# Kernel optimization log

Measured on AMD Instinct MI355X. Metric: run time of the kernel, lower is better.

The kernel has to match this reference:

```python
import jax, jax.numpy as jnp
import numpy as np

B, L, D, H = 2, 4096, 768, 12
HS = D // H  # head_size = 64
SCALE = HS ** -0.5


def setup_inputs() -> dict:
    key = jax.random.key(0)
    k1, k2, k3 = jax.random.split(key, 3)
    x = jax.random.normal(k1, (B, L, D), dtype=jnp.float32)
    # torch nn.Linear weights are [out_features, in_features]; y = x @ W.T
    Wq = jax.random.normal(k2, (D, D), dtype=jnp.float32) * (D ** -0.5)
    Wo = jax.random.normal(k3, (D, D), dtype=jnp.float32) * (D ** -0.5)
    return {"x": x, "Wq": Wq, "Wo": Wo}


def reference(x, Wq, Wo):
    b, l, d = x.shape
    # NOTE: source module uses self.query for Q, K, AND V (bug preserved).
    q = jnp.einsum('bld,ed->ble', x, Wq)              # [B,L,D]
    q = q.reshape(b, l, H, HS).transpose(0, 2, 1, 3)   # [B,H,L,HS]
    k = v = q                                          # K = V = Q (faithful)
    scores = jnp.einsum('bhqd,bhkd->bhqk', q, k) * SCALE  # [B,H,L,L]
    attn = jax.nn.softmax(scores, axis=-1)
    out = jnp.einsum('bhqk,bhkd->bhqd', attn, v)       # [B,H,L,HS]
    out = out.transpose(0, 2, 1, 3).reshape(b, l, d)   # [B,L,D]
    out = jnp.einsum('bld,ed->ble', out, Wo)           # output projection
    return out
```

## Files before the change

kernel.cpp:

```cpp
#include <hip/hip_runtime.h>
#include <hip/hip_bf16.h>

#define LQ 4096
#define DQ 768
#define NH 12
#define NB 2

typedef __attribute__((ext_vector_type(8))) short short8;
typedef __attribute__((ext_vector_type(4))) short short4v;
typedef __attribute__((ext_vector_type(2))) unsigned uint2v;
typedef __attribute__((ext_vector_type(4))) float f32x4;

__device__ __forceinline__ short f2bf(float f) {
    union { float f; unsigned u; } v; v.f = f;
    unsigned r = v.u + 0x7FFFu + ((v.u >> 16) & 1u);
    return (short)(r >> 16);
}

__device__ __forceinline__ unsigned pk2(float a, float b) {
    float2 t; t.x = a; t.y = b;
    __hip_bfloat162 h = __float22bfloat162_rn(t);
    unsigned u; __builtin_memcpy(&u, &h, 4);
    return u;
}

__device__ __forceinline__ f32x4 mfma16(short8 a, short8 b, f32x4 c) {
    return __builtin_amdgcn_mfma_f32_16x16x32_bf16(a, b, c, 0, 0, 0);
}

#define SQRT_C 0.424660f

__global__ __launch_bounds__(256) void cvtw(const float* __restrict__ a,
                                            short* __restrict__ o) {
    int i = blockIdx.x * 256 + threadIdx.x;
    float4 v = ((const float4*)a)[i];
    *(uint2v*)&o[i * 4] = (uint2v){pk2(v.x, v.y), pk2(v.z, v.w)};
}

template <int MODE>
__global__ __launch_bounds__(256, 3) void gemm_nt(const short* __restrict__ A,
                                                  const float* __restrict__ W,
                                                  void* __restrict__ Cp,
                                                  short* __restrict__ Qt) {
    __shared__ short As[128 * 72];
    __shared__ short Bs[64 * 72];
    const int t = threadIdx.x;
    const int lane = t & 63, w = t >> 6;
    const int lr = lane & 15, qd = lane >> 4;
    const int wm = (w & 1) * 64, wn = (w >> 1) * 32;
    const int lin = blockIdx.x;
    const int xcd = lin & 7, jj = lin >> 3;
    const int nt = jj % 12, mt = (jj / 12) * 8 + xcd;
    const int m0 = mt * 128, n0 = nt * 64;

    f32x4 acc[4][2];
#pragma unroll
    for (int i = 0; i < 4; ++i)
#pragma unroll
        for (int j = 0; j < 2; ++j) acc[i][j] = (f32x4){0.f, 0.f, 0.f, 0.f};

#pragma unroll
    for (int u = 0; u < 4; ++u) {
        int c = t + 256 * u, row = c >> 3, col = (c & 7) << 3;
        *(short8*)&As[row * 72 + col] = *(const short8*)&A[(size_t)(m0 + row) * DQ + col];
    }
#pragma unroll
    for (int u = 0; u < 4; ++u) {
        int c = t + 256 * u, row = c >> 4, col = (c & 15) << 2;
        float4 v = *(const float4*)&W[(size_t)(n0 + row) * DQ + col];
        *(uint2v*)&Bs[row * 72 + col] = (uint2v){pk2(v.x, v.y), pk2(v.z, v.w)};
    }
    __syncthreads();

    for (int kt = 0; kt < 12; ++kt) {
        short8 ra[4]; float4 rb[4];
        if (kt < 11) {
            const int k0 = (kt + 1) * 64;
#pragma unroll
            for (int u = 0; u < 4; ++u) {
                int c = t + 256 * u, row = c >> 3, col = (c & 7) << 3;
                ra[u] = *(const short8*)&A[(size_t)(m0 + row) * DQ + k0 + col];
            }
#pragma unroll
            for (int u = 0; u < 4; ++u) {
                int c = t + 256 * u, row = c >> 4, col = (c & 15) << 2;
                rb[u] = *(const float4*)&W[(size_t)(n0 + row) * DQ + k0 + col];
            }
        }
#pragma unroll
        for (int s = 0; s < 2; ++s) {
            short8 af[4], bf[2];
#pragma unroll
            for (int i = 0; i < 4; ++i)
                af[i] = *(short8*)&As[(wm + 16 * i + lr) * 72 + 32 * s + qd * 8];
#pragma unroll
            for (int j = 0; j < 2; ++j)
                bf[j] = *(short8*)&Bs[(wn + 16 * j + lr) * 72 + 32 * s + qd * 8];
#pragma unroll
            for (int i = 0; i < 4; ++i)
#pragma unroll
                for (int j = 0; j < 2; ++j)
                    acc[i][j] = mfma16(af[i], bf[j], acc[i][j]);
        }
        if (kt < 11) {
            __syncthreads();
#pragma unroll
            for (int u = 0; u < 4; ++u) {
                int c = t + 256 * u, row = c >> 3, col = (c & 7) << 3;
                *(short8*)&As[row * 72 + col] = ra[u];
            }
#pragma unroll
            for (int u = 0; u < 4; ++u) {
                int c = t + 256 * u, row = c >> 4, col = (c & 15) << 2;
                *(uint2v*)&Bs[row * 72 + col] = (uint2v){pk2(rb[u].x, rb[u].y), pk2(rb[u].z, rb[u].w)};
            }
            __syncthreads();
        }
    }

#pragma unroll
    for (int i = 0; i < 4; ++i)
#pragma unroll
        for (int j = 0; j < 2; ++j) {
            const int row0 = m0 + wm + 16 * i + qd * 4;
            const int col = n0 + wn + 16 * j + lr;
            if (MODE == 0) {
#pragma unroll
                for (int r = 0; r < 4; ++r)
                    ((float*)Cp)[(size_t)(row0 + r) * DQ + col] = acc[i][j][r];
            } else {
                const int b = row0 >> 12, l0 = row0 & 4095;
                const int h = col >> 6, hs = col & 63;
                const int bh = b * NH + h;
                short4v pk;
#pragma unroll
                for (int r = 0; r < 4; ++r) {
                    ((short*)Cp)[((size_t)bh * LQ + l0 + r) * 64 + hs] =
                        f2bf(acc[i][j][r] * SQRT_C);
                    pk[r] = f2bf(acc[i][j][r]);
                }
                *(short4v*)&Qt[((size_t)bh * 64 + hs) * LQ + l0] = pk;
            }
        }
}

__global__ __launch_bounds__(128, 2) void attn(const short* __restrict__ Q,
                                               const short* __restrict__ Qt,
                                               short* __restrict__ O) {
    const int linear = blockIdx.x;
    const int xcd = linear & 7, slot = linear >> 3;
    const int bh = 3 * xcd + (slot >> 5);
    const int qtile = slot & 31;
    const int t = threadIdx.x;
    const int lane = t & 63, w = t >> 6;
    const int lr = lane & 15, qd = lane >> 4;

    __shared__ short Ks[64 * 72];
    __shared__ short Vts[64 * 72];
    __shared__ short Ps[2][4][16 * 72];

    const short* Qbh = Q + (size_t)bh * LQ * 64;
    const short* Qtbh = Qt + (size_t)bh * 64 * LQ;
    const int q0 = qtile * 128 + w * 64;

    short8 aq[4][2];
#pragma unroll
    for (int i = 0; i < 4; ++i)
#pragma unroll
        for (int s = 0; s < 2; ++s)
            aq[i][s] = *(const short8*)&Qbh[(size_t)(q0 + 16 * i + lr) * 64 + 32 * s + qd * 8];

    f32x4 oacc[4][4];
#pragma unroll
    for (int i = 0; i < 4; ++i)
#pragma unroll
        for (int t2 = 0; t2 < 4; ++t2) oacc[i][t2] = (f32x4){0.f, 0.f, 0.f, 0.f};
    float l_st[4] = {0.f, 0.f, 0.f, 0.f};

#pragma unroll
    for (int u = 0; u < 4; ++u) {
        int cc = t + 128 * u;
        int row = cc >> 3, col = (cc & 7) << 3;
        *(short8*)&Ks[row * 72 + col] = *(const short8*)&Qbh[(size_t)row * 64 + col];
        *(short8*)&Vts[row * 72 + col] = *(const short8*)&Qtbh[(size_t)row * LQ + col];
    }
    __syncthreads();

    for (int kb = 0; kb < LQ / 64; ++kb) {
        short8 sk[4], sv[4];
        if (kb < LQ / 64 - 1) {
            const int k0 = (kb + 1) * 64;
#pragma unroll
            for (int u = 0; u < 4; ++u) {
                int cc = t + 128 * u;
                int row = cc >> 3, col = (cc & 7) << 3;
                sk[u] = *(const short8*)&Qbh[(size_t)(k0 + row) * 64 + col];
                sv[u] = *(const short8*)&Qtbh[(size_t)row * LQ + k0 + col];
            }
        }

        short8 kf[4][2];
#pragma unroll
        for (int t4 = 0; t4 < 4; ++t4)
#pragma unroll
            for (int s = 0; s < 2; ++s)
                kf[t4][s] = *(short8*)&Ks[(16 * t4 + lr) * 72 + 32 * s + qd * 8];

#pragma unroll
        for (int i = 0; i < 4; ++i) {
            f32x4 sacc[4];
#pragma unroll
            for (int t4 = 0; t4 < 4; ++t4) {
                sacc[t4] = (f32x4){0.f, 0.f, 0.f, 0.f};
#pragma unroll
                for (int s = 0; s < 2; ++s)
                    sacc[t4] = mfma16(kf[t4][s], aq[i][s], sacc[t4]);
            }
#pragma unroll
            for (int t4 = 0; t4 < 4; ++t4) {
                float p0 = __builtin_amdgcn_exp2f(sacc[t4][0]);
                float p1 = __builtin_amdgcn_exp2f(sacc[t4][1]);
                float p2 = __builtin_amdgcn_exp2f(sacc[t4][2]);
                float p3 = __builtin_amdgcn_exp2f(sacc[t4][3]);
                l_st[i] += (p0 + p1) + (p2 + p3);
                *(uint2v*)&Ps[w][i][lr * 72 + 16 * t4 + 4 * qd] =
                    (uint2v){pk2(p0, p1), pk2(p2, p3)};
            }
        }

#pragma unroll
        for (int ks = 0; ks < 2; ++ks) {
            short8 vb[4];
#pragma unroll
            for (int t2 = 0; t2 < 4; ++t2)
                vb[t2] = *(short8*)&Vts[(16 * t2 + lr) * 72 + 32 * ks + qd * 8];
#pragma unroll
            for (int i = 0; i < 4; ++i) {
                short8 pa = *(short8*)&Ps[w][i][lr * 72 + 32 * ks + qd * 8];
#pragma unroll
                for (int t2 = 0; t2 < 4; ++t2)
                    oacc[i][t2] = mfma16(pa, vb[t2], oacc[i][t2]);
            }
        }

        if (kb < LQ / 64 - 1) {
            __syncthreads();
#pragma unroll
            for (int u = 0; u < 4; ++u) {
                int cc = t + 128 * u;
                int row = cc >> 3, col = (cc & 7) << 3;
                *(short8*)&Ks[row * 72 + col] = sk[u];
                *(short8*)&Vts[row * 72 + col] = sv[u];
            }
            __syncthreads();
        }
    }

    const int b = bh / NH, h = bh % NH;
#pragma unroll
    for (int i = 0; i < 4; ++i) {
        float l = l_st[i];
        l += __shfl_xor(l, 16);
        l += __shfl_xor(l, 32);
        float inv[4];
#pragma unroll
        for (int r = 0; r < 4; ++r)
            inv[r] = 1.0f / __shfl(l, qd * 4 + r);
#pragma unroll
        for (int t2 = 0; t2 < 4; ++t2)
#pragma unroll
            for (int r = 0; r < 4; ++r) {
                int lq = q0 + 16 * i + qd * 4 + r;
                int e = h * 64 + 16 * t2 + lr;
                O[((size_t)(b * LQ + lq)) * DQ + e] = f2bf(oacc[i][t2][r] * inv[r]);
            }
    }
}

extern "C" void kernel_launch(void* const* d_in, const int* in_sizes, int n_in,
                              void* d_out, int out_size, void* d_ws, size_t ws_size,
                              hipStream_t stream) {
    (void)in_sizes; (void)n_in; (void)out_size; (void)ws_size;
    const float* x  = (const float*)d_in[0];
    const float* Wq = (const float*)d_in[1];
    const float* Wo = (const float*)d_in[2];
    float* out = (float*)d_out;

    const size_t NQ = (size_t)NB * NH * LQ * 64;
    short* Qws  = (short*)d_ws;
    short* Qtws = Qws  + NQ;
    short* Ows  = Qtws + NQ;

    cvtw<<<(NB * LQ * DQ) / 1024, 256, 0, stream>>>(x, Ows);
    gemm_nt<1><<<768, 256, 0, stream>>>(Ows, Wq, Qws, Qtws);
    attn<<<768, 128, 0, stream>>>(Qws, Qtws, Ows);
    gemm_nt<0><<<768, 256, 0, stream>>>(Ows, Wo, out, nullptr);
}
```

Before: 268.1 us.

## Pre-swizzle Q/V into MFMA fragment layout and drop LDS staging in attention

The Q-projection epilogue now stages its output through LDS and writes Q and V directly in MFMA-fragment-ordered blocks, replacing the row-major Q plus transposed Qt stores. The attention kernel loads K and V fragments straight from global memory into registers with a one-block prefetch of K, which removes the shared-memory K/V tiles and their two barriers per iteration. It also moves to 256 threads with 32 queries per wave, and the softmax scale is applied inside exp2 instead of being prescaled into Q. Every wave now fetches the full K/V blocks from global memory or L2 rather than sharing them through LDS, which raises cache traffic and register pressure.

```diff
diff --git a/kernel.cpp b/kernel.cpp
--- a/kernel.cpp
+++ b/kernel.cpp
@@ -7,7 +7,6 @@
 #define NB 2
 
 typedef __attribute__((ext_vector_type(8))) short short8;
-typedef __attribute__((ext_vector_type(4))) short short4v;
 typedef __attribute__((ext_vector_type(2))) unsigned uint2v;
 typedef __attribute__((ext_vector_type(4))) float f32x4;
 
@@ -28,8 +27,6 @@
     return __builtin_amdgcn_mfma_f32_16x16x32_bf16(a, b, c, 0, 0, 0);
 }
 
-#define SQRT_C 0.424660f
-
 __global__ __launch_bounds__(256) void cvtw(const float* __restrict__ a,
                                             short* __restrict__ o) {
     int i = blockIdx.x * 256 + threadIdx.x;
@@ -37,11 +34,12 @@
     *(uint2v*)&o[i * 4] = (uint2v){pk2(v.x, v.y), pk2(v.z, v.w)};
 }
 
+
 template <int MODE>
 __global__ __launch_bounds__(256, 3) void gemm_nt(const short* __restrict__ A,
                                                   const float* __restrict__ W,
                                                   void* __restrict__ Cp,
-                                                  short* __restrict__ Qt) {
+                                                  short* __restrict__ Vf) {
     __shared__ short As[128 * 72];
     __shared__ short Bs[64 * 72];
     const int t = threadIdx.x;
@@ -118,34 +116,65 @@
         }
     }
 
-#pragma unroll
-    for (int i = 0; i < 4; ++i)
-#pragma unroll
-        for (int j = 0; j < 2; ++j) {
-            const int row0 = m0 + wm + 16 * i + qd * 4;
-            const int col = n0 + wn + 16 * j + lr;
-            if (MODE == 0) {
+    if (MODE == 0) {
+#pragma unroll
+        for (int i = 0; i < 4; ++i)
+#pragma unroll
+            for (int j = 0; j < 2; ++j) {
+                const int row0 = m0 + wm + 16 * i + qd * 4;
+                const int col = n0 + wn + 16 * j + lr;
 #pragma unroll
                 for (int r = 0; r < 4; ++r)
                     ((float*)Cp)[(size_t)(row0 + r) * DQ + col] = acc[i][j][r];
-            } else {
-                const int b = row0 >> 12, l0 = row0 & 4095;
-                const int h = col >> 6, hs = col & 63;
-                const int bh = b * NH + h;
-                short4v pk;
+            }
+    } else {
+        short* Qf = (short*)Cp;
+        short* F = As;
+        const int bh = (m0 >> 12) * NH + nt;
+        const size_t gbase = (size_t)bh * (LQ * 64) + (size_t)(((m0 & 4095) >> 6) << 12);
+        __syncthreads();
+#pragma unroll
+        for (int i = 0; i < 4; ++i)
+#pragma unroll
+            for (int j = 0; j < 2; ++j) {
+                const int kl = wm + 16 * i + qd * 4;
+                const int hs = wn + 16 * j + lr;
+                const int fi = ((kl >> 6) << 12) + ((((hs >> 4) << 1) + ((kl >> 5) & 1)) << 9)
+                             + (((hs & 15) + (((kl >> 3) & 3) << 4)) << 3) + (kl & 7);
+                *(uint2v*)&F[fi] = (uint2v){pk2(acc[i][j][0], acc[i][j][1]),
+                                            pk2(acc[i][j][2], acc[i][j][3])};
+            }
+        __syncthreads();
+#pragma unroll
+        for (int p = 0; p < 4; ++p) {
+            int u = t + 256 * p;
+            *(short8*)&Vf[gbase + (size_t)u * 8] = *(short8*)&F[u * 8];
+        }
+        __syncthreads();
+#pragma unroll
+        for (int i = 0; i < 4; ++i)
+#pragma unroll
+            for (int j = 0; j < 2; ++j) {
+                const int hs = wn + 16 * j + lr;
 #pragma unroll
                 for (int r = 0; r < 4; ++r) {
-                    ((short*)Cp)[((size_t)bh * LQ + l0 + r) * 64 + hs] =
-                        f2bf(acc[i][j][r] * SQRT_C);
-                    pk[r] = f2bf(acc[i][j][r]);
+                    const int key = wm + 16 * i + qd * 4 + r;
+                    const int fi = ((key >> 6) << 12) + (((((key >> 4) & 3) << 1) + (hs >> 5)) << 9)
+                                 + (((qd * 4 + r) + (((hs >> 3) & 3) << 4)) << 3) + (hs & 7);
+                    F[fi] = f2bf(acc[i][j][r]);
                 }
-                *(short4v*)&Qt[((size_t)bh * 64 + hs) * LQ + l0] = pk;
-            }
-        }
-}
-
-__global__ __launch_bounds__(128, 2) void attn(const short* __restrict__ Q,
-                                               const short* __restrict__ Qt,
+            }
+        __syncthreads();
+#pragma unroll
+        for (int p = 0; p < 4; ++p) {
+            int u = t + 256 * p;
+            *(short8*)&Qf[gbase + (size_t)u * 8] = *(short8*)&F[u * 8];
+        }
+    }
+}
+
+__global__ __launch_bounds__(256, 3) void attn(const short* __restrict__ Qf,
+                                               const short* __restrict__ Vf,
                                                short* __restrict__ O) {
     const int linear = blockIdx.x;
     const int xcd = linear & 7, slot = linear >> 3;
@@ -155,59 +184,55 @@
     const int lane = t & 63, w = t >> 6;
     const int lr = lane & 15, qd = lane >> 4;
 
-    __shared__ short Ks[64 * 72];
-    __shared__ short Vts[64 * 72];
-    __shared__ short Ps[2][4][16 * 72];
-
-    const short* Qbh = Q + (size_t)bh * LQ * 64;
-    const short* Qtbh = Qt + (size_t)bh * 64 * LQ;
-    const int q0 = qtile * 128 + w * 64;
-
-    short8 aq[4][2];
-#pragma unroll
-    for (int i = 0; i < 4; ++i)
+    __shared__ short Ps[4][2][16 * 72];
+
+    const short* Qbh = Qf + (size_t)bh * (LQ * 64);
+    const short* Vbh = Vf + (size_t)bh * (LQ * 64);
+    const int q0 = qtile * 128 + w * 32;
+
+    short8 aq[2][2];
+#pragma unroll
+    for (int i = 0; i < 2; ++i) {
+        const int g = (q0 >> 4) + i;
 #pragma unroll
         for (int s = 0; s < 2; ++s)
-            aq[i][s] = *(const short8*)&Qbh[(size_t)(q0 + 16 * i + lr) * 64 + 32 * s + qd * 8];
-
-    f32x4 oacc[4][4];
-#pragma unroll
-    for (int i = 0; i < 4; ++i)
+            aq[i][s] = *(const short8*)&Qbh[g * 1024 + s * 512 + lane * 8];
+    }
+
+    f32x4 oacc[2][4];
+#pragma unroll
+    for (int i = 0; i < 2; ++i)
 #pragma unroll
         for (int t2 = 0; t2 < 4; ++t2) oacc[i][t2] = (f32x4){0.f, 0.f, 0.f, 0.f};
-    float l_st[4] = {0.f, 0.f, 0.f, 0.f};
-
-#pragma unroll
-    for (int u = 0; u < 4; ++u) {
-        int cc = t + 128 * u;
-        int row = cc >> 3, col = (cc & 7) << 3;
-        *(short8*)&Ks[row * 72 + col] = *(const short8*)&Qbh[(size_t)row * 64 + col];
-        *(short8*)&Vts[row * 72 + col] = *(const short8*)&Qtbh[(size_t)row * LQ + col];
-    }
-    __syncthreads();
+    float l_st[2] = {0.f, 0.f};
+
+    const float c = 0.125f * 1.44269504088896f;
+
+    short8 kf[4][2];
+#pragma unroll
+    for (int t4 = 0; t4 < 4; ++t4)
+#pragma unroll
+        for (int s = 0; s < 2; ++s)
+            kf[t4][s] = *(const short8*)&Qbh[(t4 * 2 + s) * 512 + lane * 8];
 
     for (int kb = 0; kb < LQ / 64; ++kb) {
-        short8 sk[4], sv[4];
+        short8 vb[4][2];
+#pragma unroll
+        for (int t2 = 0; t2 < 4; ++t2)
+#pragma unroll
+            for (int ks = 0; ks < 2; ++ks)
+                vb[t2][ks] = *(const short8*)&Vbh[kb * 4096 + (t2 * 2 + ks) * 512 + lane * 8];
+        short8 kfn[4][2];
         if (kb < LQ / 64 - 1) {
-            const int k0 = (kb + 1) * 64;
-#pragma unroll
-            for (int u = 0; u < 4; ++u) {
-                int cc = t + 128 * u;
-                int row = cc >> 3, col = (cc & 7) << 3;
-                sk[u] = *(const short8*)&Qbh[(size_t)(k0 + row) * 64 + col];
-                sv[u] = *(const short8*)&Qtbh[(size_t)row * LQ + k0 + col];
-            }
-        }
-
-        short8 kf[4][2];
-#pragma unroll
-        for (int t4 = 0; t4 < 4; ++t4)
-#pragma unroll
-            for (int s = 0; s < 2; ++s)
-                kf[t4][s] = *(short8*)&Ks[(16 * t4 + lr) * 72 + 32 * s + qd * 8];
-
-#pragma unroll
-        for (int i = 0; i < 4; ++i) {
+#pragma unroll
+            for (int t4 = 0; t4 < 4; ++t4)
+#pragma unroll
+                for (int s = 0; s < 2; ++s)
+                    kfn[t4][s] = *(const short8*)&Qbh[(kb + 1) * 4096 + (t4 * 2 + s) * 512 + lane * 8];
+        }
+
+#pragma unroll
+        for (int i = 0; i < 2; ++i) {
             f32x4 sacc[4];
 #pragma unroll
             for (int t4 = 0; t4 < 4; ++t4) {
@@ -218,47 +243,31 @@
             }
 #pragma unroll
             for (int t4 = 0; t4 < 4; ++t4) {
-                float p0 = __builtin_amdgcn_exp2f(sacc[t4][0]);
-                float p1 = __builtin_amdgcn_exp2f(sacc[t4][1]);
-                float p2 = __builtin_amdgcn_exp2f(sacc[t4][2]);
-                float p3 = __builtin_amdgcn_exp2f(sacc[t4][3]);
+                float p0 = __builtin_amdgcn_exp2f(sacc[t4][0] * c);
+                float p1 = __builtin_amdgcn_exp2f(sacc[t4][1] * c);
+                float p2 = __builtin_amdgcn_exp2f(sacc[t4][2] * c);
+                float p3 = __builtin_amdgcn_exp2f(sacc[t4][3] * c);
                 l_st[i] += (p0 + p1) + (p2 + p3);
                 *(uint2v*)&Ps[w][i][lr * 72 + 16 * t4 + 4 * qd] =
                     (uint2v){pk2(p0, p1), pk2(p2, p3)};
             }
-        }
-
-#pragma unroll
-        for (int ks = 0; ks < 2; ++ks) {
-            short8 vb[4];
-#pragma unroll
-            for (int t2 = 0; t2 < 4; ++t2)
-                vb[t2] = *(short8*)&Vts[(16 * t2 + lr) * 72 + 32 * ks + qd * 8];
-#pragma unroll
-            for (int i = 0; i < 4; ++i) {
+#pragma unroll
+            for (int ks = 0; ks < 2; ++ks) {
                 short8 pa = *(short8*)&Ps[w][i][lr * 72 + 32 * ks + qd * 8];
 #pragma unroll
                 for (int t2 = 0; t2 < 4; ++t2)
-                    oacc[i][t2] = mfma16(pa, vb[t2], oacc[i][t2]);
-            }
-        }
-
-        if (kb < LQ / 64 - 1) {
-            __syncthreads();
-#pragma unroll
-            for (int u = 0; u < 4; ++u) {
-                int cc = t + 128 * u;
-                int row = cc >> 3, col = (cc & 7) << 3;
-                *(short8*)&Ks[row * 72 + col] = sk[u];
-                *(short8*)&Vts[row * 72 + col] = sv[u];
-            }
-            __syncthreads();
-        }
+                    oacc[i][t2] = mfma16(pa, vb[t2][ks], oacc[i][t2]);
+            }
+        }
+#pragma unroll
+        for (int t4 = 0; t4 < 4; ++t4)
+#pragma unroll
+            for (int s = 0; s < 2; ++s) kf[t4][s] = kfn[t4][s];
     }
 
     const int b = bh / NH, h = bh % NH;
 #pragma unroll
-    for (int i = 0; i < 4; ++i) {
+    for (int i = 0; i < 2; ++i) {
         float l = l_st[i];
         l += __shfl_xor(l, 16);
         l += __shfl_xor(l, 32);
@@ -287,12 +296,12 @@
     float* out = (float*)d_out;
 
     const size_t NQ = (size_t)NB * NH * LQ * 64;
-    short* Qws  = (short*)d_ws;
-    short* Qtws = Qws  + NQ;
-    short* Ows  = Qtws + NQ;
+    short* Qf  = (short*)d_ws;
+    short* Vfb = Qf + NQ;
+    short* Ows = Vfb + NQ;
 
     cvtw<<<(NB * LQ * DQ) / 1024, 256, 0, stream>>>(x, Ows);
-    gemm_nt<1><<<768, 256, 0, stream>>>(Ows, Wq, Qws, Qtws);
-    attn<<<768, 128, 0, stream>>>(Qws, Qtws, Ows);
+    gemm_nt<1><<<768, 256, 0, stream>>>(Ows, Wq, Qf, Vfb);
+    attn<<<768, 256, 0, stream>>>(Qf, Vfb, Ows);
     gemm_nt<0><<<768, 256, 0, stream>>>(Ows, Wo, out, nullptr);
 }
```

After: 257.9 us. -3.8%, faster.
